# Optimization experiments

Hardware: AMD Instinct MI355X
Metric: run time of the kernel (lower is better)

The kernel has to match this reference:

```python
import jax, jax.numpy as jnp
import numpy as np

N = 512   # particles
T = 128   # timesteps
V_L = 3.4
V_0 = 4.2
GAMMA = 0.9
ALPHA = 0.15
BETA = 15.0
E_CRIT_INV = 2e-5
F_STD = 0.05
G_STD = 0.02
NU = 1.0 / (G_STD * float(np.sqrt(2.0 * np.pi)))
CUR_MIN = 0.0
CUR_MAX = 1.0


def voc(soc):
    # open-circuit voltage model
    return (V_L + (V_0 - V_L) * jnp.exp(GAMMA * (soc - 1.0))
            + ALPHA * V_L * (soc - 1.0)
            + (1.0 - ALPHA) * V_L * (jnp.exp(-BETA) - jnp.exp(-BETA * jnp.sqrt(soc))))


def mlp(x, w1, b1, w2, b2, w3, b3):
    h = jax.nn.sigmoid(x @ w1 + b1)
    h = jax.nn.sigmoid(h @ w2 + b2)
    return h @ w3 + b3


def setup_inputs() -> dict:
    key = jax.random.key(0)
    ks = jax.random.split(key, 11)
    soc_init = jax.random.uniform(ks[0], (N, 1), jnp.float32, 0.6, 1.0)
    current = jax.random.uniform(ks[1], (1, T), jnp.float32)
    voltage_measured = 3.4 + 0.8 * jax.random.uniform(ks[2], (1, T), jnp.float32)
    noise = jax.random.normal(ks[3], (T, N, 1), jnp.float32)
    u = jax.random.uniform(ks[4], (T,), jnp.float32)
    w1 = jax.random.normal(ks[5], (2, 1024), jnp.float32) / np.float32(np.sqrt(2.0))
    b1 = jnp.zeros((1024,), jnp.float32)
    w2 = jax.random.normal(ks[6], (1024, 512), jnp.float32) / np.float32(np.sqrt(1024.0))
    b2 = jnp.zeros((512,), jnp.float32)
    w3 = jax.random.normal(ks[7], (512, 1), jnp.float32) / np.float32(np.sqrt(512.0))
    b3 = jnp.zeros((1,), jnp.float32)
    return {"soc_init": soc_init, "current": current, "voltage_measured": voltage_measured,
            "noise": noise, "u": u, "w1": w1, "b1": b1, "w2": w2, "b2": b2, "w3": w3, "b3": b3}


def reference(soc_init, current, voltage_measured, noise, u, w1, b1, w2, b2, w3, b3):
    n = soc_init.shape[0]
    # pre-loop step: V at t=0 conditions
    I0 = current[0, 0] * jnp.ones_like(soc_init)
    sI0 = (I0 - CUR_MIN) / (CUR_MAX - CUR_MIN)
    Z0 = mlp(jnp.concatenate([soc_init, sI0], axis=1), w1, b1, w2, b2, w3, b3)
    V0 = voc(soc_init) - I0 * Z0

    log_n = jnp.log(jnp.float32(n))

    def step(carry, xs):
        soc, I, V = carry
        cur_t, vmeas_t, noise_t, u_t = xs
        # state propagation with process noise, then clamp to (0, 1]
        soc = soc - I * V * E_CRIT_INV + F_STD * noise_t
        soc = jnp.where(soc > 1.0, 1.0, jnp.where(soc < 0.0, 1e-10, soc))
        I = cur_t * jnp.ones_like(soc)
        sI = (I - CUR_MIN) / (CUR_MAX - CUR_MIN)
        Z = mlp(jnp.concatenate([soc, sI], axis=1), w1, b1, w2, b2, w3, b3)  # [N,1]
        V = voc(soc) - I * Z                                                 # [N,1]
        # importance weights / step loss (logsumexp trick as in source)
        logW = jnp.log(jnp.float32(NU)) - 0.5 * jnp.square((V - vmeas_t) / G_STD)
        step_loss = jax.nn.logsumexp(logW) - log_n
        # systematic resampling on normalized weights
        wn = jax.nn.softmax(logW[:, 0])          # normalized weights [N]
        cum = jnp.cumsum(wn)
        pos = (jnp.arange(n, dtype=jnp.float32) + u_t) / jnp.float32(n)
        idx = jnp.clip(jnp.searchsorted(cum, pos), 0, n - 1)
        soc_r = soc[idx]
        return (soc_r, I, V), (V[:, 0], soc_r[:, 0], step_loss)

    xs = (current[0], voltage_measured[0], noise, u)
    _, (v_hist, s_hist, losses) = jax.lax.scan(step, (soc_init, I0, V0), xs)
    loss = jnp.sum(losses)
    voltage = v_hist.T    # [N, T]
    soc_hist = s_hist.T   # [N, T]
    return loss, voltage, soc_hist
```

## Files before the change

### kernel.cpp

```cpp
#include <hip/hip_runtime.h>
#include <math.h>

#define NP 512
#define TS 128
#define GI 33
#define TAB2D (GI * GI)
#define GV 193
#define V_Lc 3.4f
#define V_0c 4.2f
#define GAMMAc 0.9f
#define ALPHAc 0.15f
#define BETAc 15.0f
#define E_INV 2e-5f
#define F_STDc 0.05f
#define G_STDc 0.02f

#define LBAR() asm volatile("s_waitcnt lgkmcnt(0)\n\ts_barrier" ::: "memory")

__device__ __forceinline__ float sigmoid_jax(float x) {
    float e = expf(-fabsf(x));
    float num = (x >= 0.f) ? 1.f : e;
    return num / (1.f + e);
}

__device__ __forceinline__ float vocf(float s) {
    float sm1 = s - 1.f;
    return V_Lc + (V_0c - V_Lc) * expf(GAMMAc * sm1)
         + (ALPHAc * V_Lc) * sm1
         + (1.f - ALPHAc) * V_Lc * (expf(-BETAc) - expf(-BETAc * sqrtf(s)));
}

template <int R>
__device__ __forceinline__ int dpp_ror(int v) {
    return __builtin_amdgcn_update_dpp(0, v, 0x120 | R, 0xf, 0xf, false);
}
template <int S>
__device__ __forceinline__ int dpp_shr(int v) {
    return __builtin_amdgcn_update_dpp(0, v, 0x110 | S, 0xf, 0xf, true);
}
__device__ __forceinline__ float rdlane_f(float v, int l) {
    return __int_as_float(__builtin_amdgcn_readlane(__float_as_int(v), l));
}

__device__ __forceinline__ float wave_max_f(float v) {
    v = fmaxf(v, __int_as_float(dpp_ror<1>(__float_as_int(v))));
    v = fmaxf(v, __int_as_float(dpp_ror<2>(__float_as_int(v))));
    v = fmaxf(v, __int_as_float(dpp_ror<4>(__float_as_int(v))));
    v = fmaxf(v, __int_as_float(dpp_ror<8>(__float_as_int(v))));
    int iv = __float_as_int(v);
    v = fmaxf(v, __int_as_float(__builtin_amdgcn_update_dpp(iv, iv, 0x142, 0xf, 0xf, false)));
    iv = __float_as_int(v);
    v = fmaxf(v, __int_as_float(__builtin_amdgcn_update_dpp(iv, iv, 0x143, 0xf, 0xf, false)));
    return rdlane_f(v, 63);
}

__device__ __forceinline__ int wave_max_i(int v) {
    v = max(v, dpp_ror<1>(v));
    v = max(v, dpp_ror<2>(v));
    v = max(v, dpp_ror<4>(v));
    v = max(v, dpp_ror<8>(v));
    v = max(v, __builtin_amdgcn_update_dpp(v, v, 0x142, 0xf, 0xf, false));
    v = max(v, __builtin_amdgcn_update_dpp(v, v, 0x143, 0xf, 0xf, false));
    return __builtin_amdgcn_readlane(v, 63);
}

__device__ __forceinline__ float wave_scan_add(float v, int lane) {
    v += __int_as_float(dpp_shr<1>(__float_as_int(v)));
    v += __int_as_float(dpp_shr<2>(__float_as_int(v)));
    v += __int_as_float(dpp_shr<4>(__float_as_int(v)));
    v += __int_as_float(dpp_shr<8>(__float_as_int(v)));
    float s15 = rdlane_f(v, 15);
    float s31 = rdlane_f(v, 31);
    float s47 = rdlane_f(v, 47);
    int row = lane >> 4;
    if (row >= 1) v += s15;
    if (row >= 2) v += s31;
    if (row >= 3) v += s47;
    return v;
}

__device__ __forceinline__ int wave_scanmax_i(int v, int lane) {
    v = max(v, dpp_shr<1>(v));
    v = max(v, dpp_shr<2>(v));
    v = max(v, dpp_shr<4>(v));
    v = max(v, dpp_shr<8>(v));
    int r15 = __builtin_amdgcn_readlane(v, 15);
    int r31 = __builtin_amdgcn_readlane(v, 31);
    int r47 = __builtin_amdgcn_readlane(v, 47);
    int row = lane >> 4;
    if (row >= 1) v = max(v, r15);
    if (row >= 2) v = max(v, r31);
    if (row >= 3) v = max(v, r47);
    return v;
}

__device__ __forceinline__ float interp33(const float* __restrict__ row, float s) {
    float x = s * 32.0f;
    int j = (int)floorf(x);
    j = j < 0 ? 0 : (j > 31 ? 31 : j);
    int st = j - 1;
    st = st < 0 ? 0 : (st > 29 ? 29 : st);
    float uu = x - (float)st;
    float um0 = uu, um1 = uu - 1.f, um2 = uu - 2.f, um3 = uu - 3.f;
    float c0 = um1 * um2 * um3 * (-1.f / 6.f);
    float c1 = um0 * um2 * um3 * (0.5f);
    float c2 = um0 * um1 * um3 * (-0.5f);
    float c3 = um0 * um1 * um2 * (1.f / 6.f);
    return c0 * row[st] + c1 * row[st + 1] + c2 * row[st + 2] + c3 * row[st + 3];
}

__device__ __forceinline__ float interp193(const float* __restrict__ row, float s) {
    float x = s * 192.0f;
    int j = (int)floorf(x);
    j = j < 0 ? 0 : (j > 191 ? 191 : j);
    int st = j - 1;
    st = st < 0 ? 0 : (st > 189 ? 189 : st);
    float uu = x - (float)st;
    float um0 = uu, um1 = uu - 1.f, um2 = uu - 2.f, um3 = uu - 3.f;
    float c0 = um1 * um2 * um3 * (-1.f / 6.f);
    float c1 = um0 * um2 * um3 * (0.5f);
    float c2 = um0 * um1 * um3 * (-0.5f);
    float c3 = um0 * um1 * um2 * (1.f / 6.f);
    return c0 * row[st] + c1 * row[st + 1] + c2 * row[st + 2] + c3 * row[st + 3];
}

__device__ __forceinline__ int count_le(float C, float u) {
    int h = (int)floorf(C - u);
    h = h < -1 ? -1 : (h > 511 ? 511 : h);
    h += (int)((h < 511) && (((float)(h + 1) + u) <= C));
    h -= (int)((h >= 0) && (((float)h + u) > C));
    return h + 1;
}

#define BKT 32
__global__ __launch_bounds__(256) void k_tab(
    const float* __restrict__ w1, const float* __restrict__ b1,
    const float* __restrict__ w2, const float* __restrict__ b2,
    const float* __restrict__ w3, float* __restrict__ zpart)
{
    const int tid = threadIdx.x;
    const int rowblk = blockIdx.x >> 1;
    const int colhalf = blockIdx.x & 1;
    const int r0 = rowblk * 16;
    const int cbase = colhalf * 256;

    __shared__ float As[16][BKT + 1];
    __shared__ float Bs[BKT][256];
    __shared__ float srow[16], irow[16];

    if (tid < 16) {
        int r = r0 + tid;
        r = r > (TAB2D - 1) ? (TAB2D - 1) : r;
        int si = r / GI;
        int ii = r - si * GI;
        srow[tid] = (float)si * (1.0f / 32.0f);
        irow[tid] = (float)ii * (1.0f / 32.0f);
    }
    __syncthreads();

    const int rg = tid >> 5;
    const int ct = tid & 31;
    float acc[2][8];
    #pragma unroll
    for (int a = 0; a < 2; ++a)
        #pragma unroll
        for (int b = 0; b < 8; ++b) acc[a][b] = 0.f;

    for (int kk = 0; kk < 1024; kk += BKT) {
        #pragma unroll
        for (int h = 0; h < 2; ++h) {
            int idx = tid + h * 256;
            int row = idx >> 5, k = idx & 31, kc = kk + k;
            float pre = srow[row] * w1[kc] + irow[row] * w1[1024 + kc] + b1[kc];
            As[row][k] = sigmoid_jax(pre);
        }
        #pragma unroll
        for (int jj = 0; jj < 8; ++jj) {
            int vi = tid + jj * 256;
            int k = vi >> 6, c4 = vi & 63;
            *(float4*)&Bs[k][c4 * 4] = *(const float4*)&w2[(kk + k) * 512 + cbase + c4 * 4];
        }
        __syncthreads();
        #pragma unroll
        for (int k = 0; k < BKT; ++k) {
            float a0 = As[rg * 2][k];
            float a1 = As[rg * 2 + 1][k];
            float bq[8];
            *(float4*)&bq[0] = *(const float4*)&Bs[k][ct * 4];
            *(float4*)&bq[4] = *(const float4*)&Bs[k][ct * 4 + 128];
            #pragma unroll
            for (int q = 0; q < 8; ++q) {
                acc[0][q] += a0 * bq[q];
                acc[1][q] += a1 * bq[q];
            }
        }
        __syncthreads();
    }

    float b2r[8], w3r[8];
    *(float4*)&b2r[0] = *(const float4*)&b2[cbase + ct * 4];
    *(float4*)&b2r[4] = *(const float4*)&b2[cbase + ct * 4 + 128];
    *(float4*)&w3r[0] = *(const float4*)&w3[cbase + ct * 4];
    *(float4*)&w3r[4] = *(const float4*)&w3[cbase + ct * 4 + 128];
    #pragma unroll
    for (int rr = 0; rr < 2; ++rr) {
        float zp = 0.f;
        #pragma unroll
        for (int q = 0; q < 8; ++q)
            zp += w3r[q] * sigmoid_jax(acc[rr][q] + b2r[q]);
        #pragma unroll
        for (int mm = 1; mm < 32; mm <<= 1) zp += __shfl_xor(zp, mm);
        if (ct == 0 && (r0 + rg * 2 + rr) < TAB2D)
            zpart[colhalf * TAB2D + r0 + rg * 2 + rr] = zp;
    }
}

__global__ __launch_bounds__(512, 1) void k_seq(
    const float* __restrict__ zpart, const float* __restrict__ soc_init,
    const float* __restrict__ current, const float* __restrict__ vmeas,
    const float* __restrict__ u, const float* __restrict__ noise,
    const float* __restrict__ b3, float* __restrict__ vbuf,
    float* __restrict__ sbuf, float* __restrict__ out)
{
    const int tid = threadIdx.x;
    const int lane = tid & 63;
    const int wv = tid >> 6;

    __shared__ float vt[TS][GV];
    __shared__ float zt[TS][GI];
    __shared__ float zt2d[TAB2D];
    __shared__ float vocs[GV];
    __shared__ float socs[2][NP];
    __shared__ int marker[NP];
    __shared__ float cur_s[TS], vm_s[TS], u_s[TS];
    __shared__ float2 redMT[8];

    float bb3 = b3[0];
    for (int j = tid; j < TAB2D; j += 512) zt2d[j] = zpart[j] + zpart[TAB2D + j] + bb3;
    if (tid < TS) { cur_s[tid] = current[tid]; vm_s[tid] = vmeas[tid]; u_s[tid] = u[tid]; }
    if (tid < GV) vocs[tid] = vocf((float)tid * (1.0f / 192.0f));
    marker[tid] = 0;
    __syncthreads();
    for (int idx = tid; idx < TS * GI; idx += 512) {
        int t = idx / GI, g = idx - t * GI;
        zt[t][g] = interp33(&zt2d[g * GI], cur_s[t]);
    }
    __syncthreads();
    for (int idx = tid; idx < TS * GV; idx += 512) {
        int t = idx / GV, j = idx - t * GV;
        float sj = (float)j * (1.0f / 192.0f);
        vt[t][j] = vocs[j] - cur_s[t] * interp33(&zt[t][0], sj);
    }
    __syncthreads();

    float soc = soc_init[tid];
    float Iprev = cur_s[0];
    float V = interp193(&vt[0][0], soc);
    float loss_acc = 0.f;
    const float LOG_NU = logf(19.947114020071635f);
    const float LOG_N = logf(512.f);
    float nz_cur = noise[tid];

    for (int t = 0; t < TS; ++t) {
        int tn = (t + 1 < TS) ? t + 1 : t;
        float nz_next = noise[tn * 512 + tid];

        soc = soc - Iprev * V * E_INV + F_STDc * nz_cur;
        soc = soc > 1.f ? 1.f : (soc < 0.f ? 1e-10f : soc);
        socs[t & 1][tid] = soc;

        V = interp193(&vt[t][0], soc);
        vbuf[t * 512 + tid] = V;
        float d = (V - vm_s[t]) * (1.f / G_STDc);
        float lw = LOG_NU - 0.5f * d * d;

        float m = wave_max_f(lw);
        float e = __expf(lw - m);
        float incl = wave_scan_add(e, lane);
        if (lane == 63) redMT[wv] = make_float2(m, incl);
        LBAR();

        float2 rmt = redMT[lane & 7];
        float rm = rmt.x;
        float rt = rmt.y;
        float M = rm;
        M = fmaxf(M, __int_as_float(dpp_ror<1>(__float_as_int(M))));
        M = fmaxf(M, __int_as_float(dpp_ror<2>(__float_as_int(M))));
        M = fmaxf(M, __int_as_float(dpp_ror<4>(__float_as_int(M))));
        float fw = __expf(rm - M);
        float term = rt * fw;
        float sc = term;
        sc += __int_as_float(dpp_shr<1>(__float_as_int(sc)));
        sc += __int_as_float(dpp_shr<2>(__float_as_int(sc)));
        sc += __int_as_float(dpp_shr<4>(__float_as_int(sc)));
        float S = rdlane_f(sc, 7);
        float off = 0.f;
        if (wv > 0) off = rdlane_f(sc, wv - 1);
        float fw_own = rdlane_f(fw, wv);
        loss_acc += M + __logf(S) - LOG_N;

        float C = 512.f * ((off + incl * fw_own) / S);
        int hi = count_le(C, u_s[t]);
        if (hi < 512) atomicMax(&marker[hi], (t << 10) | (tid + 1));
        LBAR();

        int pm = 0;
        for (int w = 0; w < wv; ++w) pm = max(pm, marker[w * 64 + lane]);
        pm = wave_max_i(pm);
        int v = wave_scanmax_i(marker[tid], lane);
        int sv = max(v, pm);
        int owner = ((sv >> 10) == t) ? (sv & 1023) : 0;
        owner = owner > 511 ? 511 : owner;
        float socr = socs[t & 1][owner];

        sbuf[t * 512 + tid] = socr;
        soc = socr;
        Iprev = cur_s[t];
        nz_cur = nz_next;
    }
    if (tid == 0) out[0] = loss_acc;
}

__global__ __launch_bounds__(256) void k_fin(
    const float* __restrict__ vbuf, const float* __restrict__ sbuf,
    float* __restrict__ out)
{
    __shared__ float tile[32][33];
    int tz = blockIdx.z;
    int t0 = blockIdx.x * 32;
    int i0 = blockIdx.y * 32;
    const float* src = tz ? sbuf : vbuf;
    float* dst = out + 1 + tz * (NP * TS);
    int tx = threadIdx.x & 31, ty = threadIdx.x >> 5;
    #pragma unroll
    for (int m2 = 0; m2 < 4; ++m2)
        tile[ty + 8 * m2][tx] = src[(t0 + ty + 8 * m2) * 512 + i0 + tx];
    __syncthreads();
    #pragma unroll
    for (int m2 = 0; m2 < 4; ++m2)
        dst[(i0 + ty + 8 * m2) * 128 + t0 + tx] = tile[tx][ty + 8 * m2];
}

extern "C" void kernel_launch(void* const* d_in, const int* in_sizes, int n_in,
                              void* d_out, int out_size, void* d_ws, size_t ws_size,
                              hipStream_t stream)
{
    const float* soc_init = (const float*)d_in[0];
    const float* current  = (const float*)d_in[1];
    const float* vmeas    = (const float*)d_in[2];
    const float* noise    = (const float*)d_in[3];
    const float* u        = (const float*)d_in[4];
    const float* w1 = (const float*)d_in[5];
    const float* b1 = (const float*)d_in[6];
    const float* w2 = (const float*)d_in[7];
    const float* b2 = (const float*)d_in[8];
    const float* w3 = (const float*)d_in[9];
    const float* b3 = (const float*)d_in[10];
    float* out = (float*)d_out;
    float* ws  = (float*)d_ws;

    float* zpart = ws;
    float* vbuf  = ws + 2180;
    float* sbuf  = vbuf + NP * TS;

    k_tab<<<138, 256, 0, stream>>>(w1, b1, w2, b2, w3, zpart);
    k_seq<<<1, 512, 0, stream>>>(zpart, soc_init, current, vmeas, u, noise, b3,
                                 vbuf, sbuf, out);
    k_fin<<<dim3(4, 16, 2), 256, 0, stream>>>(vbuf, sbuf, out);
}
```

Before: 259.6 us.

## Move voltage-table build to parallel kernel and process two particles per thread

The per-timestep voltage table construction moves out of the single-block sequential kernel into a new 128-block kernel that writes it to global memory; the sequential kernel then just copies it into shared memory. The sequential kernel now runs 256 threads (4 waves), each handling two particles, which shortens the cross-wave reductions and scans done at every timestep and the number of waves taking part in each barrier. The cost is an extra kernel launch, a global round-trip for the table, and more serial work per thread inside the loop.

After: 245.2 us. 1.06x faster.

```diff
diff --git a/kernel.cpp b/kernel.cpp
--- a/kernel.cpp
+++ b/kernel.cpp
@@ -215,108 +215,161 @@
     }
 }
 
-__global__ __launch_bounds__(512, 1) void k_seq(
-    const float* __restrict__ zpart, const float* __restrict__ soc_init,
+__global__ __launch_bounds__(256) void k_pre(
+    const float* __restrict__ zpart, const float* __restrict__ current,
+    const float* __restrict__ b3, float* __restrict__ vt_g)
+{
+    __shared__ float zrow[GI];
+    const int t = blockIdx.x;
+    const int tid = threadIdx.x;
+    const float It = current[t];
+    const float bb3 = b3[0];
+
+    if (tid < GI) {
+        float x = It * 32.0f;
+        int j = (int)floorf(x);
+        j = j < 0 ? 0 : (j > 31 ? 31 : j);
+        int st = j - 1;
+        st = st < 0 ? 0 : (st > 29 ? 29 : st);
+        float uu = x - (float)st;
+        float um0 = uu, um1 = uu - 1.f, um2 = uu - 2.f, um3 = uu - 3.f;
+        float c0 = um1 * um2 * um3 * (-1.f / 6.f);
+        float c1 = um0 * um2 * um3 * (0.5f);
+        float c2 = um0 * um1 * um3 * (-0.5f);
+        float c3 = um0 * um1 * um2 * (1.f / 6.f);
+        int base = tid * GI + st;
+        float n0 = zpart[base]     + zpart[TAB2D + base]     + bb3;
+        float n1 = zpart[base + 1] + zpart[TAB2D + base + 1] + bb3;
+        float n2 = zpart[base + 2] + zpart[TAB2D + base + 2] + bb3;
+        float n3 = zpart[base + 3] + zpart[TAB2D + base + 3] + bb3;
+        zrow[tid] = c0 * n0 + c1 * n1 + c2 * n2 + c3 * n3;
+    }
+    __syncthreads();
+    if (tid < GV) {
+        float sj = (float)tid * (1.0f / 192.0f);
+        vt_g[t * GV + tid] = vocf(sj) - It * interp33(zrow, sj);
+    }
+}
+
+__global__ __launch_bounds__(256, 1) void k_seq(
+    const float* __restrict__ vt_g, const float* __restrict__ soc_init,
     const float* __restrict__ current, const float* __restrict__ vmeas,
     const float* __restrict__ u, const float* __restrict__ noise,
-    const float* __restrict__ b3, float* __restrict__ vbuf,
-    float* __restrict__ sbuf, float* __restrict__ out)
+    float* __restrict__ vbuf, float* __restrict__ sbuf, float* __restrict__ out)
 {
     const int tid = threadIdx.x;
     const int lane = tid & 63;
     const int wv = tid >> 6;
 
-    __shared__ float vt[TS][GV];
-    __shared__ float zt[TS][GI];
-    __shared__ float zt2d[TAB2D];
-    __shared__ float vocs[GV];
-    __shared__ float socs[2][NP];
-    __shared__ int marker[NP];
+    __shared__ __align__(16) float vt[TS * GV];
+    __shared__ float2 socs2[2][NP / 2];
+    __shared__ int2  marker2[NP / 2];
     __shared__ float cur_s[TS], vm_s[TS], u_s[TS];
-    __shared__ float2 redMT[8];
-
-    float bb3 = b3[0];
-    for (int j = tid; j < TAB2D; j += 512) zt2d[j] = zpart[j] + zpart[TAB2D + j] + bb3;
+    __shared__ float2 redMT[4];
+    int* marker = (int*)marker2;
+
+    for (int i4 = tid; i4 < (TS * GV) / 4; i4 += 256)
+        *(float4*)&vt[i4 * 4] = *(const float4*)&vt_g[i4 * 4];
     if (tid < TS) { cur_s[tid] = current[tid]; vm_s[tid] = vmeas[tid]; u_s[tid] = u[tid]; }
-    if (tid < GV) vocs[tid] = vocf((float)tid * (1.0f / 192.0f));
-    marker[tid] = 0;
+    marker2[tid] = make_int2(0, 0);
     __syncthreads();
-    for (int idx = tid; idx < TS * GI; idx += 512) {
-        int t = idx / GI, g = idx - t * GI;
-        zt[t][g] = interp33(&zt2d[g * GI], cur_s[t]);
-    }
-    __syncthreads();
-    for (int idx = tid; idx < TS * GV; idx += 512) {
-        int t = idx / GV, j = idx - t * GV;
-        float sj = (float)j * (1.0f / 192.0f);
-        vt[t][j] = vocs[j] - cur_s[t] * interp33(&zt[t][0], sj);
-    }
-    __syncthreads();
-
-    float soc = soc_init[tid];
+
+    float2 si2 = *(const float2*)&soc_init[2 * tid];
+    float soc0 = si2.x, soc1 = si2.y;
     float Iprev = cur_s[0];
-    float V = interp193(&vt[0][0], soc);
+    float V0 = interp193(&vt[0], soc0);
+    float V1 = interp193(&vt[0], soc1);
     float loss_acc = 0.f;
     const float LOG_NU = logf(19.947114020071635f);
     const float LOG_N = logf(512.f);
-    float nz_cur = noise[tid];
+    float2 nz = *(const float2*)&noise[2 * tid];
 
     for (int t = 0; t < TS; ++t) {
         int tn = (t + 1 < TS) ? t + 1 : t;
-        float nz_next = noise[tn * 512 + tid];
-
-        soc = soc - Iprev * V * E_INV + F_STDc * nz_cur;
-        soc = soc > 1.f ? 1.f : (soc < 0.f ? 1e-10f : soc);
-        socs[t & 1][tid] = soc;
-
-        V = interp193(&vt[t][0], soc);
-        vbuf[t * 512 + tid] = V;
-        float d = (V - vm_s[t]) * (1.f / G_STDc);
-        float lw = LOG_NU - 0.5f * d * d;
-
-        float m = wave_max_f(lw);
-        float e = __expf(lw - m);
-        float incl = wave_scan_add(e, lane);
-        if (lane == 63) redMT[wv] = make_float2(m, incl);
+        float2 nz_next = *(const float2*)&noise[tn * 512 + 2 * tid];
+
+        soc0 = soc0 - Iprev * V0 * E_INV + F_STDc * nz.x;
+        soc1 = soc1 - Iprev * V1 * E_INV + F_STDc * nz.y;
+        soc0 = soc0 > 1.f ? 1.f : (soc0 < 0.f ? 1e-10f : soc0);
+        soc1 = soc1 > 1.f ? 1.f : (soc1 < 0.f ? 1e-10f : soc1);
+        socs2[t & 1][tid] = make_float2(soc0, soc1);
+
+        const float* vr = &vt[t * GV];
+        V0 = interp193(vr, soc0);
+        V1 = interp193(vr, soc1);
+        *(float2*)&vbuf[t * 512 + 2 * tid] = make_float2(V0, V1);
+        float vm = vm_s[t];
+        float d0 = (V0 - vm) * (1.f / G_STDc);
+        float d1 = (V1 - vm) * (1.f / G_STDc);
+        float lw0 = LOG_NU - 0.5f * d0 * d0;
+        float lw1 = LOG_NU - 0.5f * d1 * d1;
+
+        float m = wave_max_f(fmaxf(lw0, lw1));
+        float e0 = __expf(lw0 - m);
+        float e1 = __expf(lw1 - m);
+        float ps = wave_scan_add(e0 + e1, lane);
+        if (lane == 63) redMT[wv] = make_float2(m, ps);
         LBAR();
 
-        float2 rmt = redMT[lane & 7];
+        float2 rmt = redMT[lane & 3];
         float rm = rmt.x;
         float rt = rmt.y;
         float M = rm;
         M = fmaxf(M, __int_as_float(dpp_ror<1>(__float_as_int(M))));
         M = fmaxf(M, __int_as_float(dpp_ror<2>(__float_as_int(M))));
-        M = fmaxf(M, __int_as_float(dpp_ror<4>(__float_as_int(M))));
         float fw = __expf(rm - M);
         float term = rt * fw;
         float sc = term;
         sc += __int_as_float(dpp_shr<1>(__float_as_int(sc)));
         sc += __int_as_float(dpp_shr<2>(__float_as_int(sc)));
-        sc += __int_as_float(dpp_shr<4>(__float_as_int(sc)));
-        float S = rdlane_f(sc, 7);
-        float off = 0.f;
-        if (wv > 0) off = rdlane_f(sc, wv - 1);
+        float S = rdlane_f(sc, 3);
+        float off = (wv > 0) ? rdlane_f(sc, wv - 1) : 0.f;
         float fw_own = rdlane_f(fw, wv);
         loss_acc += M + __logf(S) - LOG_N;
 
-        float C = 512.f * ((off + incl * fw_own) / S);
-        int hi = count_le(C, u_s[t]);
-        if (hi < 512) atomicMax(&marker[hi], (t << 10) | (tid + 1));
+        float incl1 = ps;
+        float incl0 = ps - e1;
+        float C0 = 512.f * ((off + incl0 * fw_own) / S);
+        float C1 = 512.f * ((off + incl1 * fw_own) / S);
+        float ut = u_s[t];
+        int hi0 = count_le(C0, ut);
+        int hi1 = count_le(C1, ut);
+        if (hi0 < 512) atomicMax(&marker[hi0], (t << 10) | (2 * tid + 1));
+        if (hi1 < 512) atomicMax(&marker[hi1], (t << 10) | (2 * tid + 2));
         LBAR();
 
-        int pm = 0;
-        for (int w = 0; w < wv; ++w) pm = max(pm, marker[w * 64 + lane]);
-        pm = wave_max_i(pm);
-        int v = wave_scanmax_i(marker[tid], lane);
-        int sv = max(v, pm);
-        int owner = ((sv >> 10) == t) ? (sv & 1023) : 0;
-        owner = owner > 511 ? 511 : owner;
-        float socr = socs[t & 1][owner];
-
-        sbuf[t * 512 + tid] = socr;
-        soc = socr;
+        int2 mk = marker2[tid];
+        int pm_l = 0;
+        for (int w = 0; w < wv; ++w) {
+            int2 q = marker2[w * 64 + lane];
+            pm_l = max(pm_l, max(q.x, q.y));
+        }
+        int pm = wave_max_i(pm_l);
+        int mpair = max(mk.x, mk.y);
+        int psx = wave_scanmax_i(mpair, lane);
+        int up = dpp_shr<1>(psx);
+        int r15 = __builtin_amdgcn_readlane(psx, 15);
+        int r31 = __builtin_amdgcn_readlane(psx, 31);
+        int r47 = __builtin_amdgcn_readlane(psx, 47);
+        if (lane == 16) up = r15;
+        if (lane == 32) up = r31;
+        if (lane == 48) up = r47;
+        int excl = max(up, pm);
+        int tag0 = max(excl, mk.x);
+        int tag1 = max(excl, mpair);
+        int o0 = ((tag0 >> 10) == t) ? (tag0 & 1023) : 0;
+        int o1 = ((tag1 >> 10) == t) ? (tag1 & 1023) : 0;
+        o0 = o0 > 511 ? 511 : o0;
+        o1 = o1 > 511 ? 511 : o1;
+        const float* sflat = (const float*)&socs2[t & 1][0];
+        float sr0 = sflat[o0];
+        float sr1 = sflat[o1];
+        *(float2*)&sbuf[t * 512 + 2 * tid] = make_float2(sr0, sr1);
+
+        soc0 = sr0;
+        soc1 = sr1;
         Iprev = cur_s[t];
-        nz_cur = nz_next;
+        nz = nz_next;
     }
     if (tid == 0) out[0] = loss_acc;
 }
@@ -360,11 +413,13 @@
     float* ws  = (float*)d_ws;
 
     float* zpart = ws;
-    float* vbuf  = ws + 2180;
+    float* vt_g  = ws + 2180;
+    float* vbuf  = vt_g + TS * GV;
     float* sbuf  = vbuf + NP * TS;
 
     k_tab<<<138, 256, 0, stream>>>(w1, b1, w2, b2, w3, zpart);
-    k_seq<<<1, 512, 0, stream>>>(zpart, soc_init, current, vmeas, u, noise, b3,
+    k_pre<<<128, 256, 0, stream>>>(zpart, current, b3, vt_g);
+    k_seq<<<1, 256, 0, stream>>>(vt_g, soc_init, current, vmeas, u, noise,
                                  vbuf, sbuf, out);
     k_fin<<<dim3(4, 16, 2), 256, 0, stream>>>(vbuf, sbuf, out);
 }
```
